# Kernel tuning notes

Hardware: AMD Instinct MI355X
Metric: run time of the kernel (lower is better)

The kernel has to match this reference:

```python
import jax, jax.numpy as jnp
import numpy as np

N_NODES = 4096
N_EDGES = 32768
PE_DIM = 16
HIDDEN = 128


def setup_inputs() -> dict:
    key = jax.random.key(0)
    k_nodes, k_send, k_recv, k_w = jax.random.split(key, 4)
    nodes = jax.random.normal(k_nodes, (N_NODES, 8), dtype=jnp.float32)
    senders = jax.random.randint(k_send, (N_EDGES,), 0, N_NODES)
    receivers = jax.random.randint(k_recv, (N_EDGES,), 0, N_NODES)
    W = jax.random.normal(k_w, (PE_DIM, HIDDEN), dtype=jnp.float32) / np.sqrt(PE_DIM).astype(np.float32)
    b = jnp.zeros((HIDDEN,), dtype=jnp.float32)
    return {"nodes": nodes, "senders": senders, "receivers": receivers, "W": W, "b": b}


def reference(nodes, senders, receivers, W, b):
    n = nodes.shape[0]
    pe_dim = W.shape[0]
    # out-degree per node (clamped at 1, as in the original)
    ones = jnp.ones(senders.shape[0], dtype=jnp.float32)
    degree = jnp.maximum(jax.ops.segment_sum(ones, senders, num_segments=n), 1.0)
    inv_deg_e = (1.0 / degree)[senders]  # [E], per-edge 1/deg(sender)

    prob = jnp.eye(n, dtype=jnp.float32)  # [n, n] landing probabilities
    diags = []
    for _ in range(pe_dim):
        # gather sender rows, normalize, scatter-add into receiver rows
        msg = prob[senders] * inv_deg_e[:, None]           # [E, n]
        prob = jax.ops.segment_sum(msg, receivers, num_segments=n)  # [n, n]
        diags.append(jnp.diagonal(prob))                    # return probability A^k_ii
    pe = jnp.stack(diags, axis=-1)  # [n, pe_dim]
    return pe @ W + b               # [n, hidden]
```

## Files before the change

kernel.cpp:

```cpp
#include <hip/hip_runtime.h>

#define NN 4096
#define NE 32768
#define PED 16
#define HID 128
#define CW 16
#define NCHUNK 64
#define THREADS 1024
#define PASSES 4

typedef _Float16 h_t;
typedef _Float16 h8 __attribute__((ext_vector_type(8)));
typedef unsigned long long u64;

__device__ __forceinline__ int xp(int p) {
  int g = ((p & 3) << 1) | ((p >> 2) & 1);
  return ((p >> 2) << 7) | (g << 4);
}


__global__ void sort_all(const int* __restrict__ senders, const int* __restrict__ receivers,
                         float* __restrict__ dinv, int* __restrict__ indeg_g,
                         int* __restrict__ fillc,
                         int* __restrict__ rowperm, int* __restrict__ sortpos,
                         int* __restrict__ chunk_off, int* __restrict__ chunk_len) {
  __shared__ int ld_in[NN];
  __shared__ int ld_out[NN];
  __shared__ int hist[64];
  __shared__ int hbase[64];
  int t = threadIdx.x;
  for (int i = t; i < NN; i += 1024) { ld_in[i] = 0; ld_out[i] = 0; }
  if (t < 64) hist[t] = 0;
  __syncthreads();
  for (int e = t; e < NE; e += 1024) {
    atomicAdd(&ld_out[senders[e]], 1);
    atomicAdd(&ld_in[receivers[e]], 1);
  }
  __syncthreads();
  for (int r = t; r < NN; r += 1024) {
    int od = ld_out[r]; if (od < 1) od = 1;
    dinv[r] = 1.0f / (float)od;
    fillc[r] = 0;
    int d = ld_in[r]; if (d > 63) d = 63;
    indeg_g[r] = d;
    atomicAdd(&hist[d], 1);
  }
  __syncthreads();
  if (t == 0) {
    int acc = 0;
    for (int i = 0; i < 64; ++i) { hbase[i] = acc; acc += hist[i]; }
  }
  __syncthreads();
  for (int r = t; r < NN; r += 1024) {
    int d = ld_in[r]; if (d > 63) d = 63;
    int pos = atomicAdd(&hbase[d], 1);
    rowperm[pos] = r;
    sortpos[r] = pos;
  }
  __syncthreads();
  if (t < NCHUNK) {
    int m = 0;
    for (int i = 0; i < 64; ++i) {
      int rr = rowperm[(t << 6) + i];
      int d = ld_in[rr]; if (d > 63) d = 63;
      if (d > m) m = d;
    }
    chunk_len[t] = (m + 1) & ~1;
  }
  __syncthreads();
  if (t == 0) {
    int acc = 0;
    for (int c = 0; c < NCHUNK; ++c) { chunk_off[c] = acc; acc += chunk_len[c] << 6; }
    chunk_off[NCHUNK] = acc;
  }
}

__global__ void fill_ell(const int* __restrict__ senders, const int* __restrict__ receivers,
                         const int* __restrict__ sortpos, const int* __restrict__ chunk_off,
                         const float* __restrict__ dinv, int* __restrict__ fillc,
                         int2* __restrict__ ell) {
  int e = blockIdx.x * blockDim.x + threadIdx.x;
  if (e < NE) {
    int r = receivers[e], s = senders[e];
    int p = sortpos[r];
    int tslot = atomicAdd(&fillc[r], 1);
    int slot = chunk_off[p >> 6] + (tslot << 6) + (p & 63);
    ell[slot] = make_int2(xp(sortpos[s]), __float_as_int(dinv[s]));
  }
}

__global__ void sched_ell(const int* __restrict__ chunk_off,
                          const int* __restrict__ chunk_len,
                          const int* __restrict__ rowperm,
                          const int* __restrict__ indeg,
                          const int2* __restrict__ src, int2* __restrict__ dst) {
  int tid = blockIdx.x * blockDim.x + threadIdx.x;
  if (tid >= NCHUNK * 8) return;
  {
    int total = chunk_off[NCHUNK];
    for (int i = tid; i < 2048; i += 512) dst[total + i] = make_int2(0, 0);
  }
  int c = tid >> 3;
  int trk = tid & 7;
  int base = chunk_off[c];
  int len = chunk_len[c];
  int l0 = trk << 3;

  int d[8];
  u64 freeL[8];
  int dmax = 0;
#pragma unroll
  for (int j = 0; j < 8; ++j) {
    int dd = indeg[rowperm[(c << 6) + l0 + j]];
    d[j] = dd;
    if (dd > dmax) dmax = dd;
  }
  if (len > 63) {
#pragma unroll
    for (int j = 0; j < 8; ++j) {
      for (int t = 0; t < d[j]; ++t) dst[base + (t << 6) + l0 + j] = src[base + (t << 6) + l0 + j];
      for (int t = d[j]; t < len; ++t) dst[base + (t << 6) + l0 + j] = make_int2(((t + j) & 7) << 4, 0);
    }
    return;
  }
  u64 full = (len == 0) ? 0 : ((1ull << len) - 1);
#pragma unroll
  for (int j = 0; j < 8; ++j) freeL[j] = full;
  u64 fC[8];
#pragma unroll
  for (int q = 0; q < 8; ++q) fC[q] = full;

  int2 cur[8], nxt[8];
#pragma unroll
  for (int j = 0; j < 8; ++j) cur[j] = src[base + l0 + j];
  for (int t = 0; t < dmax; ++t) {
#pragma unroll
    for (int j = 0; j < 8; ++j) nxt[j] = src[base + ((t + 1) << 6) + l0 + j];
#pragma unroll
    for (int j = 0; j < 8; ++j) {
      if (t < d[j]) {
        int2 e = cur[j];
        int cls = (e.x >> 4) & 7;
        u64 fc = 0;
#pragma unroll
        for (int q = 0; q < 8; ++q) fc = (q == cls) ? fC[q] : fc;
        u64 avail = freeL[j] & fc;
        u64 pool = avail ? avail : freeL[j];
        u64 pick = pool & (~pool + 1);
        int slab = __builtin_ctzll(pick);
        freeL[j] &= ~pick;
        if (avail) {
#pragma unroll
          for (int q = 0; q < 8; ++q) if (q == cls) fC[q] &= ~pick;
        }
        dst[base + (slab << 6) + l0 + j] = e;
      }
    }
#pragma unroll
    for (int j = 0; j < 8; ++j) cur[j] = nxt[j];
  }
#pragma unroll
  for (int j = 0; j < 8; ++j) {
    u64 rem = freeL[j];
    while (rem) {
      u64 pick = rem & (~rem + 1);
      rem &= rem - 1;
      int slab = __builtin_ctzll(pick);
      int cls = 0;
#pragma unroll
      for (int q = 7; q >= 0; --q) if (fC[q] & pick) cls = q;
#pragma unroll
      for (int q = 0; q < 8; ++q) if (q == cls) fC[q] &= ~pick;
      dst[base + (slab << 6) + l0 + j] = make_int2(cls << 4, 0);
    }
  }
}


#define MIXL(acc, srcv) \
  asm("v_fma_mix_f32 %0, %1, %2, %0 op_sel_hi:[1,0,0]" : "+v"(acc) : "v"(srcv), "v"(w))
#define MIXH(acc, srcv) \
  asm("v_fma_mix_f32 %0, %1, %2, %0 op_sel:[1,0,0] op_sel_hi:[1,0,0]" : "+v"(acc) : "v"(srcv), "v"(w))

#define MIX16(lo, hi) \
  MIXL(a[0], lo.x);  MIXH(a[1], lo.x);  \
  MIXL(a[2], lo.y);  MIXH(a[3], lo.y);  \
  MIXL(a[4], lo.z);  MIXH(a[5], lo.z);  \
  MIXL(a[6], lo.w);  MIXH(a[7], lo.w);  \
  MIXL(a[8], hi.x);  MIXH(a[9], hi.x);  \
  MIXL(a[10], hi.y); MIXH(a[11], hi.y); \
  MIXL(a[12], hi.z); MIXH(a[13], hi.z); \
  MIXL(a[14], hi.w); MIXH(a[15], hi.w)

__global__ __launch_bounds__(THREADS, 4)
void fused_kernel(const int2* __restrict__ ell,
                  const int* __restrict__ chunk_off,
                  const int* __restrict__ chunk_len,
                  const int* __restrict__ rowperm,
                  float* __restrict__ pe) {
  __shared__ __align__(16) h_t X[NN * CW];
  char* Xb = (char*)X;
  int c0 = blockIdx.x * CW;
  int tid = threadIdx.x;
  int wave = tid >> 6, lane = tid & 63;

  int baseB[PASSES], lenB[PASSES], rB[PASSES], djB[PASSES], xbW[PASSES];
#pragma unroll
  for (int pass = 0; pass < PASSES; ++pass) {
    int chunk = (pass << 4) + ((pass & 1) ? (15 - wave) : wave);
    baseB[pass] = chunk_off[chunk];
    lenB[pass] = chunk_len[chunk];
    int rr = rowperm[(chunk << 6) + lane];
    rB[pass] = rr;
    djB[pass] = rr - c0;
    xbW[pass] = xp((chunk << 6) + lane);
  }

  for (int p = tid; p < NN; p += THREADS) {
    int dd = rowperm[p] - c0;
    h8 lo8, hi8;
#pragma unroll
    for (int j = 0; j < 8; ++j) {
      lo8[j] = (h_t)((dd == j) ? 1.0f : 0.0f);
      hi8[j] = (h_t)((dd == 8 + j) ? 1.0f : 0.0f);
    }
    int xb = xp(p);
    *reinterpret_cast<h8*>(Xb + xb) = lo8;
    *reinterpret_cast<h8*>(Xb + (xb ^ 16)) = hi8;
  }
  __syncthreads();

  for (int k = 0; k < PED; ++k) {
    h8 rlo[PASSES], rhi[PASSES];
#pragma unroll
    for (int pass = 0; pass < PASSES; ++pass) {
      int base = baseB[pass];
      int len = lenB[pass];
      float a[16];
#pragma unroll
      for (int j = 0; j < 16; ++j) a[j] = 0.f;
      const int2* ep = ell + base + lane;
      int2 e0 = ep[0];
      int2 e1 = ep[64];
      int2 e2 = ep[128];
      int2 e3 = ep[192];
      int4 lo0 = *reinterpret_cast<const int4*>(Xb + e0.x);
      int4 hi0 = *reinterpret_cast<const int4*>(Xb + (e0.x ^ 16));
      for (int t = 0; t < len; t += 2) {
        int2 e4 = ep[256], e5 = ep[320];
        ep += 128;
        int4 lo1 = *reinterpret_cast<const int4*>(Xb + e1.x);
        int4 hi1 = *reinterpret_cast<const int4*>(Xb + (e1.x ^ 16));
        float w = __int_as_float(e0.y);
        MIX16(lo0, hi0);
        int4 nlo = *reinterpret_cast<const int4*>(Xb + e2.x);
        int4 nhi = *reinterpret_cast<const int4*>(Xb + (e2.x ^ 16));
        w = __int_as_float(e1.y);
        MIX16(lo1, hi1);
        e0 = e2; e1 = e3; e2 = e4; e3 = e5;
        lo0 = nlo; hi0 = nhi;
      }
      h8 plo, phi;
#pragma unroll
      for (int j = 0; j < 8; ++j) { plo[j] = (h_t)a[j]; phi[j] = (h_t)a[8 + j]; }
      rlo[pass] = plo; rhi[pass] = phi;
      int dj = djB[pass];
      if (dj >= 0 && dj < CW) {
        float dv = a[0];
#pragma unroll
        for (int j = 1; j < 16; ++j) dv = (dj == j) ? a[j] : dv;
        pe[rB[pass] * PED + k] = dv;
      }
    }
    __syncthreads();
#pragma unroll
    for (int pass = 0; pass < PASSES; ++pass) {
      int xb = xbW[pass];
      *reinterpret_cast<h8*>(Xb + xb) = rlo[pass];
      *reinterpret_cast<h8*>(Xb + (xb ^ 16)) = rhi[pass];
    }
    __syncthreads();
  }
}

__global__ void out_kernel(const float* __restrict__ pe, const float* __restrict__ W,
                           const float* __restrict__ bvec, float* __restrict__ out) {
  __shared__ float sW[PED * HID];
  int r = blockIdx.x;
  int h = threadIdx.x;
  for (int i = h; i < PED * HID; i += HID) sW[i] = W[i];
  __syncthreads();
  float acc = bvec[h];
  float p[PED];
#pragma unroll
  for (int kk = 0; kk < PED; ++kk) p[kk] = pe[r * PED + kk];
#pragma unroll
  for (int kk = 0; kk < PED; ++kk) acc = fmaf(p[kk], sW[kk * HID + h], acc);
  out[r * HID + h] = acc;
}

extern "C" void kernel_launch(void* const* d_in, const int* in_sizes, int n_in,
                              void* d_out, int out_size, void* d_ws, size_t ws_size,
                              hipStream_t stream) {
  const int* senders = (const int*)d_in[1];
  const int* receivers = (const int*)d_in[2];
  const float* W = (const float*)d_in[3];
  const float* bvec = (const float*)d_in[4];
  float* out = (float*)d_out;

  char* p = (char*)d_ws;
  int* indeg = (int*)p;     p += (size_t)NN * 4;
  int* fillc = (int*)p;     p += (size_t)NN * 4;
  float* dinv = (float*)p;  p += (size_t)NN * 4;
  int* rowperm = (int*)p;   p += (size_t)NN * 4;
  int* sortpos = (int*)p;   p += (size_t)NN * 4;
  int* chunk_off = (int*)p; p += 128 * 4;
  int* chunk_len = (int*)p; p += 128 * 4;
  float* pe = (float*)p;    p += (size_t)NN * PED * 4;
  size_t ell_slots = (size_t)64 * NE + 2048;
  int2* ell = (int2*)p;     p += ell_slots * sizeof(int2);
  int2* ell2 = (int2*)p;

  sort_all<<<1, 1024, 0, stream>>>(senders, receivers, dinv, indeg, fillc,
                                   rowperm, sortpos, chunk_off, chunk_len);
  fill_ell<<<NE / 256, 256, 0, stream>>>(senders, receivers, sortpos, chunk_off, dinv, fillc, ell);
  sched_ell<<<8, 64, 0, stream>>>(chunk_off, chunk_len, rowperm, indeg, ell, ell2);

  fused_kernel<<<NN / CW, THREADS, 0, stream>>>(ell2, chunk_off, chunk_len, rowperm, pe);

  out_kernel<<<NN, HID, 0, stream>>>(pe, W, bvec, out);
}
```

Baseline: 208.1 us.

## Parallelize degree counting and fuse output projection into propagation kernel

The single-block sort kernel is split in two. Degree counting now runs as a multi-block atomic kernel after a memset, and a single-block kernel builds the row permutation. The pe@W+b projection moves into the tail of the fused propagation kernel, which keeps each block's 16 diagonal values in shared memory, so the separate output kernel and the global pe buffer go away. The final X write-back on the last step is also skipped. This adds two launches (memset plus count) in exchange for removing the serial per-edge atomics in one block and one kernel launch.

```diff
diff --git a/kernel.cpp b/kernel.cpp
--- a/kernel.cpp
+++ b/kernel.cpp
@@ -19,30 +19,33 @@
 }
 
 
-__global__ void sort_all(const int* __restrict__ senders, const int* __restrict__ receivers,
-                         float* __restrict__ dinv, int* __restrict__ indeg_g,
-                         int* __restrict__ fillc,
-                         int* __restrict__ rowperm, int* __restrict__ sortpos,
-                         int* __restrict__ chunk_off, int* __restrict__ chunk_len) {
-  __shared__ int ld_in[NN];
-  __shared__ int ld_out[NN];
+__global__ void count_kernel(const int* __restrict__ senders,
+                             const int* __restrict__ receivers,
+                             int* __restrict__ outdeg, int* __restrict__ indeg) {
+  int e = blockIdx.x * blockDim.x + threadIdx.x;
+  if (e < NE) {
+    atomicAdd(&outdeg[senders[e]], 1);
+    atomicAdd(&indeg[receivers[e]], 1);
+  }
+}
+
+__global__ void perm_kernel(const int* __restrict__ outdeg, int* __restrict__ indeg,
+                            float* __restrict__ dinv, int* __restrict__ fillc,
+                            int* __restrict__ rowperm, int* __restrict__ sortpos,
+                            int* __restrict__ chunk_off, int* __restrict__ chunk_len) {
+  __shared__ int ld_d[NN];
   __shared__ int hist[64];
   __shared__ int hbase[64];
   int t = threadIdx.x;
-  for (int i = t; i < NN; i += 1024) { ld_in[i] = 0; ld_out[i] = 0; }
   if (t < 64) hist[t] = 0;
   __syncthreads();
-  for (int e = t; e < NE; e += 1024) {
-    atomicAdd(&ld_out[senders[e]], 1);
-    atomicAdd(&ld_in[receivers[e]], 1);
-  }
-  __syncthreads();
   for (int r = t; r < NN; r += 1024) {
-    int od = ld_out[r]; if (od < 1) od = 1;
+    int od = outdeg[r]; if (od < 1) od = 1;
     dinv[r] = 1.0f / (float)od;
     fillc[r] = 0;
-    int d = ld_in[r]; if (d > 63) d = 63;
-    indeg_g[r] = d;
+    int d = indeg[r]; if (d > 63) d = 63;
+    ld_d[r] = d;
+    indeg[r] = d;
     atomicAdd(&hist[d], 1);
   }
   __syncthreads();
@@ -52,8 +55,7 @@
   }
   __syncthreads();
   for (int r = t; r < NN; r += 1024) {
-    int d = ld_in[r]; if (d > 63) d = 63;
-    int pos = atomicAdd(&hbase[d], 1);
+    int pos = atomicAdd(&hbase[ld_d[r]], 1);
     rowperm[pos] = r;
     sortpos[r] = pos;
   }
@@ -61,8 +63,7 @@
   if (t < NCHUNK) {
     int m = 0;
     for (int i = 0; i < 64; ++i) {
-      int rr = rowperm[(t << 6) + i];
-      int d = ld_in[rr]; if (d > 63) d = 63;
+      int d = ld_d[rowperm[(t << 6) + i]];
       if (d > m) m = d;
     }
     chunk_len[t] = (m + 1) & ~1;
@@ -197,22 +198,23 @@
                   const int* __restrict__ chunk_off,
                   const int* __restrict__ chunk_len,
                   const int* __restrict__ rowperm,
-                  float* __restrict__ pe) {
+                  const float* __restrict__ W,
+                  const float* __restrict__ bvec,
+                  float* __restrict__ out) {
   __shared__ __align__(16) h_t X[NN * CW];
+  __shared__ float pe_lds[CW * PED];
   char* Xb = (char*)X;
   int c0 = blockIdx.x * CW;
   int tid = threadIdx.x;
   int wave = tid >> 6, lane = tid & 63;
 
-  int baseB[PASSES], lenB[PASSES], rB[PASSES], djB[PASSES], xbW[PASSES];
+  int baseB[PASSES], lenB[PASSES], djB[PASSES], xbW[PASSES];
 #pragma unroll
   for (int pass = 0; pass < PASSES; ++pass) {
     int chunk = (pass << 4) + ((pass & 1) ? (15 - wave) : wave);
     baseB[pass] = chunk_off[chunk];
     lenB[pass] = chunk_len[chunk];
-    int rr = rowperm[(chunk << 6) + lane];
-    rB[pass] = rr;
-    djB[pass] = rr - c0;
+    djB[pass] = rowperm[(chunk << 6) + lane] - c0;
     xbW[pass] = xp((chunk << 6) + lane);
   }
 
@@ -269,34 +271,38 @@
         float dv = a[0];
 #pragma unroll
         for (int j = 1; j < 16; ++j) dv = (dj == j) ? a[j] : dv;
-        pe[rB[pass] * PED + k] = dv;
+        pe_lds[dj * PED + k] = dv;
       }
     }
-    __syncthreads();
-#pragma unroll
-    for (int pass = 0; pass < PASSES; ++pass) {
-      int xb = xbW[pass];
-      *reinterpret_cast<h8*>(Xb + xb) = rlo[pass];
-      *reinterpret_cast<h8*>(Xb + (xb ^ 16)) = rhi[pass];
-    }
-    __syncthreads();
-  }
-}
-
-__global__ void out_kernel(const float* __restrict__ pe, const float* __restrict__ W,
-                           const float* __restrict__ bvec, float* __restrict__ out) {
-  __shared__ float sW[PED * HID];
-  int r = blockIdx.x;
-  int h = threadIdx.x;
-  for (int i = h; i < PED * HID; i += HID) sW[i] = W[i];
-  __syncthreads();
-  float acc = bvec[h];
-  float p[PED];
-#pragma unroll
-  for (int kk = 0; kk < PED; ++kk) p[kk] = pe[r * PED + kk];
-#pragma unroll
-  for (int kk = 0; kk < PED; ++kk) acc = fmaf(p[kk], sW[kk * HID + h], acc);
-  out[r * HID + h] = acc;
+    if (k != PED - 1) {
+      __syncthreads();
+#pragma unroll
+      for (int pass = 0; pass < PASSES; ++pass) {
+        int xb = xbW[pass];
+        *reinterpret_cast<h8*>(Xb + xb) = rlo[pass];
+        *reinterpret_cast<h8*>(Xb + (xb ^ 16)) = rhi[pass];
+      }
+      __syncthreads();
+    }
+  }
+  __syncthreads();
+
+  {
+    int h = tid & 127;
+    int r0 = tid >> 7;
+    float wcol[PED];
+#pragma unroll
+    for (int kk = 0; kk < PED; ++kk) wcol[kk] = W[kk * HID + h];
+    float bb = bvec[h];
+#pragma unroll
+    for (int half = 0; half < 2; ++half) {
+      int row = r0 + (half << 3);
+      float acc = bb;
+#pragma unroll
+      for (int kk = 0; kk < PED; ++kk) acc = fmaf(pe_lds[row * PED + kk], wcol[kk], acc);
+      out[(size_t)(c0 + row) * HID + h] = acc;
+    }
+  }
 }
 
 extern "C" void kernel_launch(void* const* d_in, const int* in_sizes, int n_in,
@@ -309,6 +315,7 @@
   float* out = (float*)d_out;
 
   char* p = (char*)d_ws;
+  int* outdeg = (int*)p;    p += (size_t)NN * 4;
   int* indeg = (int*)p;     p += (size_t)NN * 4;
   int* fillc = (int*)p;     p += (size_t)NN * 4;
   float* dinv = (float*)p;  p += (size_t)NN * 4;
@@ -316,17 +323,16 @@
   int* sortpos = (int*)p;   p += (size_t)NN * 4;
   int* chunk_off = (int*)p; p += 128 * 4;
   int* chunk_len = (int*)p; p += 128 * 4;
-  float* pe = (float*)p;    p += (size_t)NN * PED * 4;
   size_t ell_slots = (size_t)64 * NE + 2048;
   int2* ell = (int2*)p;     p += ell_slots * sizeof(int2);
   int2* ell2 = (int2*)p;
 
-  sort_all<<<1, 1024, 0, stream>>>(senders, receivers, dinv, indeg, fillc,
-                                   rowperm, sortpos, chunk_off, chunk_len);
+  hipMemsetAsync(d_ws, 0, (size_t)NN * 4 * 2, stream);
+  count_kernel<<<NE / 256, 256, 0, stream>>>(senders, receivers, outdeg, indeg);
+  perm_kernel<<<1, 1024, 0, stream>>>(outdeg, indeg, dinv, fillc,
+                                      rowperm, sortpos, chunk_off, chunk_len);
   fill_ell<<<NE / 256, 256, 0, stream>>>(senders, receivers, sortpos, chunk_off, dinv, fillc, ell);
   sched_ell<<<8, 64, 0, stream>>>(chunk_off, chunk_len, rowperm, indeg, ell, ell2);
 
-  fused_kernel<<<NN / CW, THREADS, 0, stream>>>(ell2, chunk_off, chunk_len, rowperm, pe);
-
-  out_kernel<<<NN, HID, 0, stream>>>(pe, W, bvec, out);
-}
+  fused_kernel<<<NN / CW, THREADS, 0, stream>>>(ell2, chunk_off, chunk_len, rowperm, W, bvec, out);
+}
```

After: 206.7 us. Within noise of the previous version (-0.7%).
